# Performance work log

Measured on AMD Instinct MI355X. Metric: run time of the kernel, lower is better.

## Reference

```python
import jax, jax.numpy as jnp
import numpy as np

B, N, D = 64, 32, 512

# Off-diagonal pair indices in the exact order the torch module uses:
# k = N*i + j for i in range(N) for j in range(N) if j != i.
_pairs = [(i, j) for i in range(N) for j in range(N) if j != i]
IDX_I = jnp.asarray(np.array([p[0] for p in _pairs], dtype=np.int32))  # [N*(N-1)]
IDX_J = jnp.asarray(np.array([p[1] for p in _pairs], dtype=np.int32))


def setup_inputs() -> dict:
    key = jax.random.key(0)
    k0, k1, k2 = jax.random.split(key, 3)
    person_feats = jax.random.normal(k0, (B, N, D), dtype=jnp.float32)
    # MLP: Linear(2D -> D) -> ReLU -> Linear(D -> D); Kaiming-ish scaling.
    W1 = jax.random.normal(k1, (D, 2 * D), dtype=jnp.float32) * (1.0 / np.sqrt(2 * D))
    b1 = jnp.zeros((D,), dtype=jnp.float32)
    W2 = jax.random.normal(k2, (D, D), dtype=jnp.float32) * (1.0 / np.sqrt(D))
    b2 = jnp.zeros((D,), dtype=jnp.float32)
    return {"person_feats": person_feats, "W1": W1, "b1": b1, "W2": W2, "b2": b2}


def reference(person_feats, W1, b1, W2, b2):
    # Original math: tem1[b, N*i+j] = feats[b, i]; tem2[b, N*i+j] = feats[b, j];
    # select off-diagonal indices -> pairwise concat(feat_i, feat_j).
    # We gather the N*(N-1) needed pairs directly instead of materializing N*N.
    fi = person_feats[:, IDX_I, :]            # [B, N*(N-1), D]
    fj = person_feats[:, IDX_J, :]            # [B, N*(N-1), D]
    x = jnp.concatenate([fi, fj], axis=-1)    # [B, N*(N-1), 2D]
    h = jax.nn.relu(jnp.einsum('bpk,dk->bpd', x, W1) + b1)
    out = jnp.einsum('bpk,dk->bpd', h, W2) + b2  # [B, N*(N-1), D]
    return out
```

## Files before the change

kernel.cpp:

```cpp
#include <hip/hip_runtime.h>
#include <hip/hip_bf16.h>
#include <stdint.h>


typedef __attribute__((ext_vector_type(4))) float f32x4;
typedef __attribute__((ext_vector_type(8))) short bf16x8;
typedef __attribute__((ext_vector_type(4))) unsigned int u32x4;
typedef __attribute__((ext_vector_type(2))) unsigned int u32x2;

__device__ __forceinline__ uint32_t cvt2_bf16(float a, float b) {
    __hip_bfloat162 h = __float22bfloat162_rn(make_float2(a, b));
    uint32_t u;
    __builtin_memcpy(&u, &h, 4);
    return u;
}

__device__ __forceinline__ void async_lds16(const void* g, void* l) {
    __builtin_amdgcn_global_load_lds(
        (const __attribute__((address_space(1))) void*)g,
        (__attribute__((address_space(3))) void*)l, 16, 0, 0);
}

__global__ __launch_bounds__(256) void prep(const float* __restrict__ pf,
                                            const float* __restrict__ W1,
                                            const float* __restrict__ b1,
                                            const float* __restrict__ W2,
                                            float* __restrict__ UV,
                                            unsigned short* __restrict__ W2r) {
    __shared__ unsigned short As[64][64];
    __shared__ unsigned short Bs[128][64];

    const int t = threadIdx.x;
    const int bxg = blockIdx.x;

    if (bxg >= 256) {
        int s = (bxg - 256) * 256 + t;
        int l = s & 63;
        int fn = (s >> 6) & 31;
        int kt = s >> 11;
        int col = fn * 16 + (l & 15);
        int k = kt * 32 + (l >> 4) * 8;
        const float* src = W2 + (size_t)col * 512 + k;
        f32x4 a = ((const f32x4*)src)[0];
        f32x4 b = ((const f32x4*)src)[1];
        u32x4 P;
        P[0] = cvt2_bf16(a[0], a[1]); P[1] = cvt2_bf16(a[2], a[3]);
        P[2] = cvt2_bf16(b[0], b[1]); P[3] = cvt2_bf16(b[2], b[3]);
        *(u32x4*)(W2r + (size_t)s * 8) = P;
        return;
    }

    const int m0 = (bxg >> 3) * 64;
    const int c0 = (bxg & 7) * 128;

    const int sr = t >> 2;
    const int sk = (t & 3) << 4;
    const int g0 = (t & 3) << 1;

    const int wave = t >> 6, lane = t & 63;
    const int wr = wave >> 1, wc = wave & 1;
    const int lr = lane & 15, lkq = lane >> 4;
    const int s7 = lr & 7;

    f32x4 acc[2][4] = {};

    const float* a_src = pf + (size_t)(m0 + sr) * 512 + sk;
    const float* b_src[2];
    int wbB0[2], wbB1[2];
#pragma unroll
    for (int pass = 0; pass < 2; ++pass) {
        int c = c0 + pass * 64 + sr;
        int d = c & 511;
        int koff = (c >> 9) * 512;
        b_src[pass] = W1 + (size_t)d * 1024 + koff + sk;
        int rb = pass * 64 + sr, s = rb & 7;
        wbB0[pass] = rb * 128 + (((g0    ) ^ s) << 4);
        wbB1[pass] = rb * 128 + (((g0 + 1) ^ s) << 4);
    }
    const int sA = sr & 7;
    const int wbA0 = sr * 128 + (((g0    ) ^ sA) << 4);
    const int wbA1 = sr * 128 + (((g0 + 1) ^ sA) << 4);

    for (int kt = 0; kt < 512; kt += 64) {
        {
            const float* gp = a_src + kt;
            f32x4 x0 = ((const f32x4*)gp)[0];
            f32x4 x1 = ((const f32x4*)gp)[1];
            f32x4 x2 = ((const f32x4*)gp)[2];
            f32x4 x3 = ((const f32x4*)gp)[3];
            u32x4 P0, P1;
            P0[0] = cvt2_bf16(x0[0], x0[1]); P0[1] = cvt2_bf16(x0[2], x0[3]);
            P0[2] = cvt2_bf16(x1[0], x1[1]); P0[3] = cvt2_bf16(x1[2], x1[3]);
            P1[0] = cvt2_bf16(x2[0], x2[1]); P1[1] = cvt2_bf16(x2[2], x2[3]);
            P1[2] = cvt2_bf16(x3[0], x3[1]); P1[3] = cvt2_bf16(x3[2], x3[3]);
            *(u32x4*)((char*)&As[0][0] + wbA0) = P0;
            *(u32x4*)((char*)&As[0][0] + wbA1) = P1;
        }
#pragma unroll
        for (int pass = 0; pass < 2; ++pass) {
            const float* gp = b_src[pass] + kt;
            f32x4 x0 = ((const f32x4*)gp)[0];
            f32x4 x1 = ((const f32x4*)gp)[1];
            f32x4 x2 = ((const f32x4*)gp)[2];
            f32x4 x3 = ((const f32x4*)gp)[3];
            u32x4 P0, P1;
            P0[0] = cvt2_bf16(x0[0], x0[1]); P0[1] = cvt2_bf16(x0[2], x0[3]);
            P0[2] = cvt2_bf16(x1[0], x1[1]); P0[3] = cvt2_bf16(x1[2], x1[3]);
            P1[0] = cvt2_bf16(x2[0], x2[1]); P1[1] = cvt2_bf16(x2[2], x2[3]);
            P1[2] = cvt2_bf16(x3[0], x3[1]); P1[3] = cvt2_bf16(x3[2], x3[3]);
            *(u32x4*)((char*)&Bs[0][0] + wbB0[pass]) = P0;
            *(u32x4*)((char*)&Bs[0][0] + wbB1[pass]) = P1;
        }
        __syncthreads();
#pragma unroll
        for (int kk = 0; kk < 2; ++kk) {
            const int co = (((kk << 2) + lkq) ^ s7) << 3;
            bf16x8 af[2], bfr[4];
#pragma unroll
            for (int m = 0; m < 2; ++m)
                af[m] = *(const bf16x8*)(&As[0][0] + (wr * 32 + m * 16 + lr) * 64 + co);
#pragma unroll
            for (int n = 0; n < 4; ++n)
                bfr[n] = *(const bf16x8*)(&Bs[0][0] + (wc * 64 + n * 16 + lr) * 64 + co);
#pragma unroll
            for (int m = 0; m < 2; ++m)
#pragma unroll
                for (int n = 0; n < 4; ++n)
                    acc[m][n] = __builtin_amdgcn_mfma_f32_16x16x32_bf16(
                        af[m], bfr[n], acc[m][n], 0, 0, 0);
        }
        __syncthreads();
    }

    const int cr = lane >> 4;
    const int cc = lane & 15;
#pragma unroll
    for (int m = 0; m < 2; ++m) {
#pragma unroll
        for (int n = 0; n < 4; ++n) {
            int c = c0 + wc * 64 + n * 16 + cc;
            float bias = (c < 512) ? b1[c] : 0.0f;
            int rowb = m0 + wr * 32 + m * 16 + cr * 4;
#pragma unroll
            for (int r_ = 0; r_ < 4; ++r_)
                UV[(size_t)(rowb + r_) * 1024 + c] = acc[m][n][r_] + bias;
        }
    }
}

__global__ __launch_bounds__(256, 2) void fused_gemm(const float* __restrict__ UV,
                                                     const unsigned short* __restrict__ W2r,
                                                     const float* __restrict__ b2,
                                                     float* __restrict__ out) {
    __shared__ unsigned char As[2][4096];
    __shared__ unsigned char Bs[2][32768];

    const int t = threadIdx.x;
    const int bx = blockIdx.x;
    const int mt = (bx & 7) * 124 + (bx >> 3);
    const int m0 = mt << 6;

    const int wave = t >> 6, lane = t & 63;

    const int arow = t >> 2;
    const int ks = t & 3;
    const float* uptr;
    const float* vptr;
    {
        int m = m0 + arow;
        int b = m / 992, p = m - b * 992;
        int i = p / 31, r = p - i * 31;
        int j = r + (r >= i ? 1 : 0);
        uptr = UV + (size_t)(b * 32 + i) * 1024 + ks * 8;
        vptr = UV + (size_t)(b * 32 + j) * 1024 + 512 + ks * 8;
    }
    const int awoff = (arow >> 4) * 1024 + (ks * 16 + (arow & 15)) * 16;

    const int cr = lane >> 4;
    const int cc = lane & 15;

    f32x4 acc[8][4] = {};

#define BUILD_A(dst, U0, U1, V0, V1)                                           \
    {                                                                          \
        f32x4 h0, h1;                                                          \
        _Pragma("unroll")                                                      \
        for (int q = 0; q < 4; ++q) {                                          \
            h0[q] = fmaxf(U0[q] + V0[q], 0.0f);                                \
            h1[q] = fmaxf(U1[q] + V1[q], 0.0f);                                \
        }                                                                      \
        u32x4 P;                                                               \
        P[0] = cvt2_bf16(h0[0], h0[1]); P[1] = cvt2_bf16(h0[2], h0[3]);        \
        P[2] = cvt2_bf16(h1[0], h1[1]); P[3] = cvt2_bf16(h1[2], h1[3]);        \
        *(u32x4*)((dst) + awoff) = P;                                          \
    }

    {
        f32x4 u0 = ((const f32x4*)uptr)[0], u1 = ((const f32x4*)uptr)[1];
        f32x4 v0 = ((const f32x4*)vptr)[0], v1 = ((const f32x4*)vptr)[1];
        const char* gs = (const char*)W2r + t * 16;
#pragma unroll
        for (int q = 0; q < 8; ++q)
            async_lds16(gs + q * 4096, &Bs[0][0] + q * 4096 + wave * 1024);
        BUILD_A(&As[0][0], u0, u1, v0, v1);
    }

#pragma unroll 1
    for (int step = 0; step < 16; ++step) {
        const int buf = step & 1;
        __syncthreads();

        f32x4 u0, u1, v0, v1;
        if (step < 15) {
            const float* up = uptr + (step + 1) * 32;
            const float* vp = vptr + (step + 1) * 32;
            u0 = ((const f32x4*)up)[0]; u1 = ((const f32x4*)up)[1];
            v0 = ((const f32x4*)vp)[0]; v1 = ((const f32x4*)vp)[1];
            const char* gs = (const char*)W2r + (step + 1) * 32768 + t * 16;
#pragma unroll
            for (int q = 0; q < 8; ++q)
                async_lds16(gs + q * 4096, &Bs[buf ^ 1][0] + q * 4096 + wave * 1024);
        }

        {
            const unsigned char* aB = &As[buf][0];
            const unsigned char* bB = &Bs[buf][0];
            bf16x8 af[4], bfr[8];
#pragma unroll
            for (int m = 0; m < 4; ++m)
                af[m] = *(const bf16x8*)(aB + m * 1024 + lane * 16);
#pragma unroll
            for (int n = 0; n < 8; ++n)
                bfr[n] = *(const bf16x8*)(bB + (wave * 8 + n) * 1024 + lane * 16);
            __builtin_amdgcn_s_setprio(1);
#pragma unroll
            for (int n = 0; n < 8; ++n)
#pragma unroll
                for (int m = 0; m < 4; ++m)
                    acc[n][m] = __builtin_amdgcn_mfma_f32_16x16x32_bf16(
                        af[m], bfr[n], acc[n][m], 0, 0, 0);
            __builtin_amdgcn_s_setprio(0);
        }

        if (step < 15) {
            BUILD_A(&As[buf ^ 1][0], u0, u1, v0, v1);
        }
    }
#undef BUILD_A

#pragma unroll
    for (int n = 0; n < 8; ++n) {
        int col = wave * 128 + n * 16 + cc;
        float bias = b2[col];
#pragma unroll
        for (int m = 0; m < 4; ++m) {
            int rowb = m0 + m * 16 + cr * 4;
#pragma unroll
            for (int r_ = 0; r_ < 4; ++r_)
                out[(size_t)(rowb + r_) * 512 + col] = acc[n][m][r_] + bias;
        }
    }
}

extern "C" void kernel_launch(void* const* d_in, const int* in_sizes, int n_in,
                              void* d_out, int out_size, void* d_ws, size_t ws_size,
                              hipStream_t stream) {
    const float* pf = (const float*)d_in[0];
    const float* W1 = (const float*)d_in[1];
    const float* b1 = (const float*)d_in[2];
    const float* W2 = (const float*)d_in[3];
    const float* b2 = (const float*)d_in[4];
    float* out = (float*)d_out;

    float* UV = (float*)d_ws;
    unsigned short* W2r = (unsigned short*)((char*)d_ws + (size_t)8 * 1024 * 1024);

    prep<<<dim3(384), dim3(256), 0, stream>>>(pf, W1, b1, W2, UV, W2r);
    fused_gemm<<<dim3(992), dim3(256), 0, stream>>>(UV, W2r, b2, out);
}
```

Baseline: 80.40 us.

## Halve prep tile rows for more blocks; deepen UV prefetch in fused GEMM

The prep GEMM now uses 32-row tiles instead of 64, doubling its grid from 256 to 512 GEMM blocks so the 2048x1024 UV projection fills more compute units. The main fused GEMM loop is unrolled by two with explicit ping-pong buffers, and U/V activations are loaded two steps ahead, hiding global-load latency behind the MFMA work. The cost is more register pressure in the fused kernel and less reuse per block in prep.

After: 78.96 us. No clear change (-1.8%).

```diff
diff --git a/kernel.cpp b/kernel.cpp
--- a/kernel.cpp
+++ b/kernel.cpp
@@ -6,7 +6,6 @@
 typedef __attribute__((ext_vector_type(4))) float f32x4;
 typedef __attribute__((ext_vector_type(8))) short bf16x8;
 typedef __attribute__((ext_vector_type(4))) unsigned int u32x4;
-typedef __attribute__((ext_vector_type(2))) unsigned int u32x2;
 
 __device__ __forceinline__ uint32_t cvt2_bf16(float a, float b) {
     __hip_bfloat162 h = __float22bfloat162_rn(make_float2(a, b));
@@ -27,14 +26,14 @@
                                             const float* __restrict__ W2,
                                             float* __restrict__ UV,
                                             unsigned short* __restrict__ W2r) {
-    __shared__ unsigned short As[64][64];
+    __shared__ unsigned short As[32][64];
     __shared__ unsigned short Bs[128][64];
 
     const int t = threadIdx.x;
     const int bxg = blockIdx.x;
 
-    if (bxg >= 256) {
-        int s = (bxg - 256) * 256 + t;
+    if (bxg >= 512) {
+        int s = (bxg - 512) * 256 + t;
         int l = s & 63;
         int fn = (s >> 6) & 31;
         int kt = s >> 11;
@@ -50,84 +49,63 @@
         return;
     }
 
-    const int m0 = (bxg >> 3) * 64;
+    const int m0 = (bxg >> 3) * 32;
     const int c0 = (bxg & 7) * 128;
 
-    const int sr = t >> 2;
-    const int sk = (t & 3) << 4;
-    const int g0 = (t & 3) << 1;
+    const int row8 = t >> 3;
+    const int g = t & 7;
 
     const int wave = t >> 6, lane = t & 63;
     const int wr = wave >> 1, wc = wave & 1;
     const int lr = lane & 15, lkq = lane >> 4;
     const int s7 = lr & 7;
 
-    f32x4 acc[2][4] = {};
-
-    const float* a_src = pf + (size_t)(m0 + sr) * 512 + sk;
-    const float* b_src[2];
-    int wbB0[2], wbB1[2];
-#pragma unroll
-    for (int pass = 0; pass < 2; ++pass) {
-        int c = c0 + pass * 64 + sr;
+    f32x4 acc[4] = {};
+
+    const float* a_src = pf + (size_t)(m0 + row8) * 512 + g * 8;
+    const float* b_src[4];
+    int wbB[4];
+#pragma unroll
+    for (int p = 0; p < 4; ++p) {
+        int rb = p * 32 + row8;
+        int c = c0 + rb;
         int d = c & 511;
         int koff = (c >> 9) * 512;
-        b_src[pass] = W1 + (size_t)d * 1024 + koff + sk;
-        int rb = pass * 64 + sr, s = rb & 7;
-        wbB0[pass] = rb * 128 + (((g0    ) ^ s) << 4);
-        wbB1[pass] = rb * 128 + (((g0 + 1) ^ s) << 4);
-    }
-    const int sA = sr & 7;
-    const int wbA0 = sr * 128 + (((g0    ) ^ sA) << 4);
-    const int wbA1 = sr * 128 + (((g0 + 1) ^ sA) << 4);
+        b_src[p] = W1 + (size_t)d * 1024 + koff + g * 8;
+        wbB[p] = rb * 128 + ((g ^ (rb & 7)) << 4);
+    }
+    const int wbA = row8 * 128 + ((g ^ (row8 & 7)) << 4);
 
     for (int kt = 0; kt < 512; kt += 64) {
         {
             const float* gp = a_src + kt;
             f32x4 x0 = ((const f32x4*)gp)[0];
             f32x4 x1 = ((const f32x4*)gp)[1];
-            f32x4 x2 = ((const f32x4*)gp)[2];
-            f32x4 x3 = ((const f32x4*)gp)[3];
-            u32x4 P0, P1;
-            P0[0] = cvt2_bf16(x0[0], x0[1]); P0[1] = cvt2_bf16(x0[2], x0[3]);
-            P0[2] = cvt2_bf16(x1[0], x1[1]); P0[3] = cvt2_bf16(x1[2], x1[3]);
-            P1[0] = cvt2_bf16(x2[0], x2[1]); P1[1] = cvt2_bf16(x2[2], x2[3]);
-            P1[2] = cvt2_bf16(x3[0], x3[1]); P1[3] = cvt2_bf16(x3[2], x3[3]);
-            *(u32x4*)((char*)&As[0][0] + wbA0) = P0;
-            *(u32x4*)((char*)&As[0][0] + wbA1) = P1;
-        }
-#pragma unroll
-        for (int pass = 0; pass < 2; ++pass) {
-            const float* gp = b_src[pass] + kt;
+            u32x4 P;
+            P[0] = cvt2_bf16(x0[0], x0[1]); P[1] = cvt2_bf16(x0[2], x0[3]);
+            P[2] = cvt2_bf16(x1[0], x1[1]); P[3] = cvt2_bf16(x1[2], x1[3]);
+            *(u32x4*)((char*)&As[0][0] + wbA) = P;
+        }
+#pragma unroll
+        for (int p = 0; p < 4; ++p) {
+            const float* gp = b_src[p] + kt;
             f32x4 x0 = ((const f32x4*)gp)[0];
             f32x4 x1 = ((const f32x4*)gp)[1];
-            f32x4 x2 = ((const f32x4*)gp)[2];
-            f32x4 x3 = ((const f32x4*)gp)[3];
-            u32x4 P0, P1;
-            P0[0] = cvt2_bf16(x0[0], x0[1]); P0[1] = cvt2_bf16(x0[2], x0[3]);
-            P0[2] = cvt2_bf16(x1[0], x1[1]); P0[3] = cvt2_bf16(x1[2], x1[3]);
-            P1[0] = cvt2_bf16(x2[0], x2[1]); P1[1] = cvt2_bf16(x2[2], x2[3]);
-            P1[2] = cvt2_bf16(x3[0], x3[1]); P1[3] = cvt2_bf16(x3[2], x3[3]);
-            *(u32x4*)((char*)&Bs[0][0] + wbB0[pass]) = P0;
-            *(u32x4*)((char*)&Bs[0][0] + wbB1[pass]) = P1;
+            u32x4 P;
+            P[0] = cvt2_bf16(x0[0], x0[1]); P[1] = cvt2_bf16(x0[2], x0[3]);
+            P[2] = cvt2_bf16(x1[0], x1[1]); P[3] = cvt2_bf16(x1[2], x1[3]);
+            *(u32x4*)((char*)&Bs[0][0] + wbB[p]) = P;
         }
         __syncthreads();
 #pragma unroll
         for (int kk = 0; kk < 2; ++kk) {
             const int co = (((kk << 2) + lkq) ^ s7) << 3;
-            bf16x8 af[2], bfr[4];
-#pragma unroll
-            for (int m = 0; m < 2; ++m)
-                af[m] = *(const bf16x8*)(&As[0][0] + (wr * 32 + m * 16 + lr) * 64 + co);
-#pragma unroll
-            for (int n = 0; n < 4; ++n)
-                bfr[n] = *(const bf16x8*)(&Bs[0][0] + (wc * 64 + n * 16 + lr) * 64 + co);
-#pragma unroll
-            for (int m = 0; m < 2; ++m)
-#pragma unroll
-                for (int n = 0; n < 4; ++n)
-                    acc[m][n] = __builtin_amdgcn_mfma_f32_16x16x32_bf16(
-                        af[m], bfr[n], acc[m][n], 0, 0, 0);
+            bf16x8 af = *(const bf16x8*)(&As[0][0] + (wr * 16 + lr) * 64 + co);
+#pragma unroll
+            for (int n = 0; n < 4; ++n) {
+                bf16x8 bfr = *(const bf16x8*)(&Bs[0][0] + (wc * 64 + n * 16 + lr) * 64 + co);
+                acc[n] = __builtin_amdgcn_mfma_f32_16x16x32_bf16(af, bfr, acc[n], 0, 0, 0);
+            }
         }
         __syncthreads();
     }
@@ -135,16 +113,13 @@
     const int cr = lane >> 4;
     const int cc = lane & 15;
 #pragma unroll
-    for (int m = 0; m < 2; ++m) {
-#pragma unroll
-        for (int n = 0; n < 4; ++n) {
-            int c = c0 + wc * 64 + n * 16 + cc;
-            float bias = (c < 512) ? b1[c] : 0.0f;
-            int rowb = m0 + wr * 32 + m * 16 + cr * 4;
-#pragma unroll
-            for (int r_ = 0; r_ < 4; ++r_)
-                UV[(size_t)(rowb + r_) * 1024 + c] = acc[m][n][r_] + bias;
-        }
+    for (int n = 0; n < 4; ++n) {
+        int c = c0 + wc * 64 + n * 16 + cc;
+        float bias = (c < 512) ? b1[c] : 0.0f;
+        int rowb = m0 + wr * 16 + cr * 4;
+#pragma unroll
+        for (int r_ = 0; r_ < 4; ++r_)
+            UV[(size_t)(rowb + r_) * 1024 + c] = acc[n][r_] + bias;
     }
 }
 
@@ -181,7 +156,26 @@
 
     f32x4 acc[8][4] = {};
 
-#define BUILD_A(dst, U0, U1, V0, V1)                                           \
+    f32x4 Pu0, Pu1, Pv0, Pv1;
+    f32x4 Qu0, Qu1, Qv0, Qv1;
+
+#define DMA_B(S, DSTBUF)                                                       \
+    {                                                                          \
+        const char* gs = (const char*)W2r + (S) * 32768 + t * 16;              \
+        _Pragma("unroll")                                                      \
+        for (int q = 0; q < 8; ++q)                                            \
+            async_lds16(gs + q * 4096, &Bs[DSTBUF][0] + q * 4096 + wave * 1024);\
+    }
+
+#define LOAD_UV(S, U0, U1, V0, V1)                                             \
+    {                                                                          \
+        const float* up = uptr + (S) * 32;                                     \
+        const float* vp = vptr + (S) * 32;                                     \
+        U0 = ((const f32x4*)up)[0]; U1 = ((const f32x4*)up)[1];                \
+        V0 = ((const f32x4*)vp)[0]; V1 = ((const f32x4*)vp)[1];                \
+    }
+
+#define BUILD_A(DSTBUF, U0, U1, V0, V1)                                        \
     {                                                                          \
         f32x4 h0, h1;                                                          \
         _Pragma("unroll")                                                      \
@@ -192,61 +186,53 @@
         u32x4 P;                                                               \
         P[0] = cvt2_bf16(h0[0], h0[1]); P[1] = cvt2_bf16(h0[2], h0[3]);        \
         P[2] = cvt2_bf16(h1[0], h1[1]); P[3] = cvt2_bf16(h1[2], h1[3]);        \
-        *(u32x4*)((dst) + awoff) = P;                                          \
-    }
-
-    {
-        f32x4 u0 = ((const f32x4*)uptr)[0], u1 = ((const f32x4*)uptr)[1];
-        f32x4 v0 = ((const f32x4*)vptr)[0], v1 = ((const f32x4*)vptr)[1];
-        const char* gs = (const char*)W2r + t * 16;
-#pragma unroll
-        for (int q = 0; q < 8; ++q)
-            async_lds16(gs + q * 4096, &Bs[0][0] + q * 4096 + wave * 1024);
-        BUILD_A(&As[0][0], u0, u1, v0, v1);
-    }
+        *(u32x4*)(&As[DSTBUF][0] + awoff) = P;                                 \
+    }
+
+#define MFMA_STEP(BUF)                                                         \
+    {                                                                          \
+        const unsigned char* aB = &As[BUF][0];                                 \
+        const unsigned char* bB = &Bs[BUF][0];                                 \
+        bf16x8 af[4], bfr[8];                                                  \
+        _Pragma("unroll")                                                      \
+        for (int m = 0; m < 4; ++m)                                            \
+            af[m] = *(const bf16x8*)(aB + m * 1024 + lane * 16);               \
+        _Pragma("unroll")                                                      \
+        for (int n = 0; n < 8; ++n)                                            \
+            bfr[n] = *(const bf16x8*)(bB + (wave * 8 + n) * 1024 + lane * 16); \
+        __builtin_amdgcn_s_setprio(1);                                         \
+        _Pragma("unroll")                                                      \
+        for (int n = 0; n < 8; ++n)                                            \
+            _Pragma("unroll")                                                  \
+            for (int m = 0; m < 4; ++m)                                        \
+                acc[n][m] = __builtin_amdgcn_mfma_f32_16x16x32_bf16(           \
+                    af[m], bfr[n], acc[n][m], 0, 0, 0);                        \
+        __builtin_amdgcn_s_setprio(0);                                         \
+    }
+
+    DMA_B(0, 0);
+    LOAD_UV(0, Pu0, Pu1, Pv0, Pv1);
+    LOAD_UV(1, Qu0, Qu1, Qv0, Qv1);
+    BUILD_A(0, Pu0, Pu1, Pv0, Pv1);
 
 #pragma unroll 1
-    for (int step = 0; step < 16; ++step) {
-        const int buf = step & 1;
-        __syncthreads();
-
-        f32x4 u0, u1, v0, v1;
-        if (step < 15) {
-            const float* up = uptr + (step + 1) * 32;
-            const float* vp = vptr + (step + 1) * 32;
-            u0 = ((const f32x4*)up)[0]; u1 = ((const f32x4*)up)[1];
-            v0 = ((const f32x4*)vp)[0]; v1 = ((const f32x4*)vp)[1];
-            const char* gs = (const char*)W2r + (step + 1) * 32768 + t * 16;
-#pragma unroll
-            for (int q = 0; q < 8; ++q)
-                async_lds16(gs + q * 4096, &Bs[buf ^ 1][0] + q * 4096 + wave * 1024);
-        }
-
-        {
-            const unsigned char* aB = &As[buf][0];
-            const unsigned char* bB = &Bs[buf][0];
-            bf16x8 af[4], bfr[8];
-#pragma unroll
-            for (int m = 0; m < 4; ++m)
-                af[m] = *(const bf16x8*)(aB + m * 1024 + lane * 16);
-#pragma unroll
-            for (int n = 0; n < 8; ++n)
-                bfr[n] = *(const bf16x8*)(bB + (wave * 8 + n) * 1024 + lane * 16);
-            __builtin_amdgcn_s_setprio(1);
-#pragma unroll
-            for (int n = 0; n < 8; ++n)
-#pragma unroll
-                for (int m = 0; m < 4; ++m)
-                    acc[n][m] = __builtin_amdgcn_mfma_f32_16x16x32_bf16(
-                        af[m], bfr[n], acc[n][m], 0, 0, 0);
-            __builtin_amdgcn_s_setprio(0);
-        }
-
-        if (step < 15) {
-            BUILD_A(&As[buf ^ 1][0], u0, u1, v0, v1);
-        }
-    }
+    for (int s2 = 0; s2 < 16; s2 += 2) {
+        __syncthreads();
+        DMA_B(s2 + 1, 1);
+        if (s2 < 14) LOAD_UV(s2 + 2, Pu0, Pu1, Pv0, Pv1);
+        MFMA_STEP(0);
+        BUILD_A(1, Qu0, Qu1, Qv0, Qv1);
+
+        __syncthreads();
+        if (s2 < 14) DMA_B(s2 + 2, 0);
+        if (s2 < 14) LOAD_UV(s2 + 3, Qu0, Qu1, Qv0, Qv1);
+        MFMA_STEP(1);
+        if (s2 < 14) BUILD_A(0, Pu0, Pu1, Pv0, Pv1);
+    }
+#undef DMA_B
+#undef LOAD_UV
 #undef BUILD_A
+#undef MFMA_STEP
 
 #pragma unroll
     for (int n = 0; n < 8; ++n) {
@@ -275,6 +261,6 @@
     float* UV = (float*)d_ws;
     unsigned short* W2r = (unsigned short*)((char*)d_ws + (size_t)8 * 1024 * 1024);
 
-    prep<<<dim3(384), dim3(256), 0, stream>>>(pf, W1, b1, W2, UV, W2r);
+    prep<<<dim3(640), dim3(256), 0, stream>>>(pf, W1, b1, W2, UV, W2r);
     fused_gemm<<<dim3(992), dim3(256), 0, stream>>>(UV, W2r, b2, out);
 }
```
